# Kernel optimization log

Hardware: AMD Instinct MI355X
Metric: run time of the kernel (lower is better)

## Reference

```python
import jax, jax.numpy as jnp
import numpy as np
from jax import lax

R = 1
EPS = 1e-4
K = 2 * R + 1


def _dir_kernels(r):
    k = 2 * r + 1
    ones = np.ones((k, k), np.float32)
    L = ones.copy(); L[:, r + 1:] = 0
    Rk = ones.copy(); Rk[:, :r] = 0
    U = ones.copy(); U[r + 1:, :] = 0
    D = ones.copy(); D[:r, :] = 0
    # NW/NE/SW/SE clone U/D BEFORE normalization (as in the torch code)
    NW = U.copy(); NW[:, r + 1:] = 0
    NE = U.copy(); NE[:, :r] = 0
    SW = D.copy(); SW[:, r + 1:] = 0
    SE = D.copy(); SE[:, :r] = 0
    half = (r + 1) * k          # normalizer for half windows
    quad = (r + 1) ** 2         # normalizer for quadrant windows
    L, Rk, U, D = L / half, Rk / half, U / half, D / half
    NW, NE, SW, SE = NW / quad, NE / quad, SW / quad, SE / quad
    return jnp.asarray(np.stack([L, Rk, U, D, NW, NE, SW, SE])[:, None])  # [8,1,k,k]


_DN = ('NCHW', 'OIHW', 'NCHW')


def _boxfilter(x, r):
    # replication pad + depthwise ones/(k*k) box filter; x: [N,3,H,W]
    k = 2 * r + 1
    xp = jnp.pad(x, ((0, 0), (0, 0), (r, r), (r, r)), mode='edge')
    w = jnp.full((3, 1, k, k), 1.0 / (k * k), dtype=x.dtype)
    return lax.conv_general_dilated(xp, w, (1, 1), 'VALID',
                                    dimension_numbers=_DN, feature_group_count=3)


def setup_inputs() -> dict:
    key = jax.random.key(0)
    k1, k2, k3 = jax.random.split(key, 3)
    lr_x = jax.random.uniform(k1, (1, 3, 2048, 2048), jnp.float32) * 255.0
    lr_y = jax.random.uniform(k2, (1, 3, 2048, 2048), jnp.float32) * 255.0
    hr_x = jax.random.uniform(k3, (1, 3, 4096, 4096), jnp.float32) * 255.0
    return {"lr_x": lr_x, "lr_y": lr_y, "hr_x": hr_x}


def reference(lr_x, lr_y, hr_x):
    # guided-filter coefficients on the low-res pair
    mean_x = _boxfilter(lr_x, R)
    mean_y = _boxfilter(lr_y, R)
    cov_xy = _boxfilter(lr_x * lr_y, R) - mean_x * mean_y
    var_x = _boxfilter(lr_x * lr_x, R) - mean_x * mean_x
    A = cov_xy / (var_x + EPS)            # [1,3,H,W]
    b = mean_y - A * mean_x               # [1,3,H,W]

    # treat channels as batch: [3,1,H,W]; 8 directional kernels at once
    Wd = _dir_kernels(R)                  # [8,1,k,k]
    A_ = A[0][:, None]
    b_ = b[0][:, None]
    im = lr_x[0][:, None]                 # [3,1,H,W]
    pad = [(R, R), (R, R)]
    convA = lax.conv_general_dilated(A_, Wd, (1, 1), pad, dimension_numbers=_DN)
    convb = lax.conv_general_dilated(b_, Wd, (1, 1), pad, dimension_numbers=_DN)
    d = convA * im + convb - im           # [3,8,H,W] directional residuals

    idx = jnp.argmin(jnp.abs(d), axis=1, keepdims=True)   # [3,1,H,W]
    dm = jnp.take_along_axis(d, idx, axis=1)              # best residual
    res = (dm + im).transpose(1, 0, 2, 3)                 # [1,3,H,W]
    # .int() truncation then clamp to [0,255], back to float
    return jnp.clip(jnp.trunc(res), 0.0, 255.0)
```

## Files before the change

### kernel.cpp

```cpp
#include <hip/hip_runtime.h>
#include <math.h>


#define BX 512
#define TY 16
#define NT 256

__device__ __forceinline__ double fast_rcp(double v) {
#if __has_builtin(__builtin_amdgcn_rcp)
    double r = __builtin_amdgcn_rcp(v);
#else
    double r = 1.0 / v;
#endif
    double e = fma(-v, r, 1.0);
    r = fma(r, e, r);
    e = fma(-v, r, 1.0);
    r = fma(r, e, r);
    return r;
}

__device__ __forceinline__ int iclamp(int v, int lo, int hi) {
    return v < lo ? lo : (v > hi ? hi : v);
}

template <int P, bool EMIT, bool PREF>
__device__ __forceinline__ void fgf_step(
    int S, int y0, int c0, int H, int W,
    const float* __restrict__ xc, const float* __restrict__ yc,
    float* __restrict__ oc,
    const int (&coli)[6], const bool (&av)[4],
    float (&xr)[3][6], float (&yr)[3][6],
    float (&xn)[6], float (&yn)[6],
    double (&CA)[3][2][3], double (&CB)[3][2][3])
{
    const double EPS81 = 81.0 * 1.0e-4;
    const double INV9  = 1.0 / 9.0;
    const double I6    = 1.0 / 6.0;
    constexpr int PO = (P + 1) % 3;
    constexpr int PM = (P + 2) % 3;

#pragma unroll
    for (int k = 0; k < 6; k++) { xr[P][k] = xn[k]; yr[P][k] = yn[k]; }

    if (PREF) {
        int rn = y0 + S + 1; if (rn > H - 1) rn = H - 1;
        const float* __restrict__ pxn = xc + (size_t)rn * W;
        const float* __restrict__ pyn = yc + (size_t)rn * W;
#pragma unroll
        for (int k = 0; k < 6; k++) { xn[k] = pxn[coli[k]]; yn[k] = pyn[coli[k]]; }
    }

    const int ar = y0 + S - 1;

    double Sx[6], Sy[6], Sxy[6], Sxx[6];
#pragma unroll
    for (int k = 0; k < 6; k++) {
        double x0v = (double)xr[PO][k];
        double x1v = (double)xr[PM][k];
        double x2v = (double)xr[P][k];
        double y0v = (double)yr[PO][k];
        double y1v = (double)yr[PM][k];
        double y2v = (double)yr[P][k];
        Sx[k]  = (x0v + x1v) + x2v;
        Sy[k]  = (y0v + y1v) + y2v;
        Sxy[k] = fma(x2v, y2v, fma(x1v, y1v, x0v * y0v));
        Sxx[k] = fma(x2v, x2v, fma(x1v, x1v, x0v * x0v));
    }

    const bool rvalid = (ar >= 0) && (ar < H);
    double Aj[4], Bj[4];
#pragma unroll
    for (int j = 0; j < 4; j++) {
        double sx3  = (Sx[j]  + Sx[j + 1])  + Sx[j + 2];
        double sy3  = (Sy[j]  + Sy[j + 1])  + Sy[j + 2];
        double sxy3 = (Sxy[j] + Sxy[j + 1]) + Sxy[j + 2];
        double sxx3 = (Sxx[j] + Sxx[j + 1]) + Sxx[j + 2];
        double num = fma(9.0, sxy3, -(sx3 * sy3));
        double den = fma(-sx3, sx3, fma(9.0, sxx3, EPS81));
        double Av = num * fast_rcp(den);
        double Bv = fma(-Av, sx3, sy3) * INV9;
        bool ok = rvalid && av[j];
        Aj[j] = ok ? Av : 0.0;
        Bj[j] = ok ? Bv : 0.0;
    }

#pragma unroll
    for (int i = 0; i < 2; i++) {
        double l = Aj[i] + Aj[i + 1], r = Aj[i + 1] + Aj[i + 2];
        CA[P][i][0] = l; CA[P][i][1] = r; CA[P][i][2] = l + Aj[i + 2];
        l = Bj[i] + Bj[i + 1]; r = Bj[i + 1] + Bj[i + 2];
        CB[P][i][0] = l; CB[P][i][1] = r; CB[P][i][2] = l + Bj[i + 2];
    }

    if (EMIT) {
        const int oy = ar - 1;
        if (oy < H) {
            float o0 = 0.0f, o1 = 0.0f;
#pragma unroll
            for (int i = 0; i < 2; i++) {
                double im  = (double)xr[PO][i + 2];
                double mim = -im;
                double nwA = CA[PO][i][0] + CA[PM][i][0];
                double neA = CA[PO][i][1] + CA[PM][i][1];
                double sa[8] = {
                    nwA + CA[P][i][0],
                    neA + CA[P][i][1],
                    CA[PO][i][2] + CA[PM][i][2],
                    CA[PM][i][2] + CA[P][i][2],
                    nwA,
                    neA,
                    CA[PM][i][0] + CA[P][i][0],
                    CA[PM][i][1] + CA[P][i][1]
                };
                double nwB = CB[PO][i][0] + CB[PM][i][0];
                double neB = CB[PO][i][1] + CB[PM][i][1];
                double sb[8] = {
                    nwB + CB[P][i][0],
                    neB + CB[P][i][1],
                    CB[PO][i][2] + CB[PM][i][2],
                    CB[PM][i][2] + CB[P][i][2],
                    nwB,
                    neB,
                    CB[PM][i][0] + CB[P][i][0],
                    CB[PM][i][1] + CB[P][i][1]
                };
                double best = 0.0;
#pragma unroll
                for (int q = 0; q < 8; q++) {
                    double wq = (q < 4) ? I6 : 0.25;
                    double dq = fma(wq, fma(sa[q], im, sb[q]), mim);
                    if (q == 0) best = dq;
                    else best = (fabs(dq) < fabs(best)) ? dq : best;
                }
                double res = trunc(best + im);
                res = fmin(fmax(res, 0.0), 255.0);
                if (i == 0) o0 = (float)res; else o1 = (float)res;
            }
            size_t ob = (size_t)oy * W + c0;
            if (c0 + 1 < W) {
                float2 o2; o2.x = o0; o2.y = o1;
                *reinterpret_cast<float2*>(&oc[ob]) = o2;
            } else if (c0 < W) {
                oc[ob] = o0;
            }
        }
    }
}

__global__ __launch_bounds__(NT, 2) void fgf_band_kernel(
    const float* __restrict__ x, const float* __restrict__ y,
    float* __restrict__ out, int H, int W)
{
    const int c   = blockIdx.z;
    const int bx0 = blockIdx.x * BX;
    const int y0  = blockIdx.y * TY;
    const size_t plane = (size_t)H * (size_t)W;
    const float* xc = x + (size_t)c * plane;
    const float* yc = y + (size_t)c * plane;
    float* oc = out + (size_t)c * plane;

    const int t  = threadIdx.y * 64 + threadIdx.x;
    const int c0 = bx0 + 2 * t;

    int coli[6];
    bool av[4];
#pragma unroll
    for (int k = 0; k < 6; k++) coli[k] = iclamp(c0 - 2 + k, 0, W - 1);
#pragma unroll
    for (int j = 0; j < 4; j++) { int ax = c0 - 1 + j; av[j] = (ax >= 0) && (ax < W); }

    float  xr[3][6], yr[3][6], xn[6], yn[6];
    double CA[3][2][3], CB[3][2][3];

    {
        int r1 = iclamp(y0 - 2, 0, H - 1);
        int r2 = iclamp(y0 - 1, 0, H - 1);
        const float* px1 = xc + (size_t)r1 * W;  const float* py1 = yc + (size_t)r1 * W;
        const float* px2 = xc + (size_t)r2 * W;  const float* py2 = yc + (size_t)r2 * W;
        const float* px3 = xc + (size_t)y0 * W;  const float* py3 = yc + (size_t)y0 * W;
#pragma unroll
        for (int k = 0; k < 6; k++) {
            xr[1][k] = px1[coli[k]]; yr[1][k] = py1[coli[k]];
            xr[2][k] = px2[coli[k]]; yr[2][k] = py2[coli[k]];
            xn[k]    = px3[coli[k]]; yn[k]    = py3[coli[k]];
        }
    }

    fgf_step<0, false, true>(0, y0, c0, H, W, xc, yc, oc, coli, av, xr, yr, xn, yn, CA, CB);
    fgf_step<1, false, true>(1, y0, c0, H, W, xc, yc, oc, coli, av, xr, yr, xn, yn, CA, CB);
#pragma unroll 1
    for (int sb = 0; sb < 5; sb++) {
        const int S2 = 2 + 3 * sb;
        fgf_step<2, true, true>(S2,     y0, c0, H, W, xc, yc, oc, coli, av, xr, yr, xn, yn, CA, CB);
        fgf_step<0, true, true>(S2 + 1, y0, c0, H, W, xc, yc, oc, coli, av, xr, yr, xn, yn, CA, CB);
        fgf_step<1, true, true>(S2 + 2, y0, c0, H, W, xc, yc, oc, coli, av, xr, yr, xn, yn, CA, CB);
    }
    fgf_step<2, true, false>(17, y0, c0, H, W, xc, yc, oc, coli, av, xr, yr, xn, yn, CA, CB);
}

extern "C" void kernel_launch(void* const* d_in, const int* in_sizes, int n_in,
                              void* d_out, int out_size, void* d_ws, size_t ws_size,
                              hipStream_t stream) {
    const float* lr_x = (const float*)d_in[0];
    const float* lr_y = (const float*)d_in[1];
    float* out = (float*)d_out;

    const int plane = in_sizes[0] / 3;
    const int H = (int)(0.5 + sqrt((double)plane));
    const int W = plane / H;

    dim3 block(64, 4, 1);
    dim3 grid((W + BX - 1) / BX, (H + TY - 1) / TY, 3);
    fgf_band_kernel<<<grid, block, 0, stream>>>(lr_x, lr_y, out, H, W);
}
```

Baseline: 348.4 us.

## Map one column per lane and share horizontal sums via DPP row shifts

Each lane now handles a single column, and the horizontal 3-tap sums of the box statistics and the A/B coefficients come from neighbouring lanes through DPP row-shift moves. Before, each thread loaded six columns and recomputed the overlapping sums itself. This removes redundant loads and fp64 arithmetic, but each 64-lane wave emits only 60 output columns because of halo lanes. The band height grows from 16 to 30 rows and the occupancy hint rises to 3, so the redundant halo rows are amortised over more outputs at the cost of more serial work per block.

```diff
diff --git a/kernel.cpp b/kernel.cpp
--- a/kernel.cpp
+++ b/kernel.cpp
@@ -2,8 +2,9 @@
 #include <math.h>
 
 
-#define BX 512
-#define TY 16
+#define WCOLS 60
+#define BCOLS (4 * WCOLS)
+#define TY 30
 #define NT 256
 
 __device__ __forceinline__ double fast_rcp(double v) {
@@ -23,15 +24,25 @@
     return v < lo ? lo : (v > hi ? hi : v);
 }
 
+template <int CTRL>
+__device__ __forceinline__ double dpp_mov64(double v) {
+    int lo = __double2loint(v);
+    int hi = __double2hiint(v);
+    lo = __builtin_amdgcn_mov_dpp(lo, CTRL, 0xF, 0xF, true);
+    hi = __builtin_amdgcn_mov_dpp(hi, CTRL, 0xF, 0xF, true);
+    return __hiloint2double(hi, lo);
+}
+__device__ __forceinline__ double nbr_left(double v)  { return dpp_mov64<0x138>(v); }
+__device__ __forceinline__ double nbr_right(double v) { return dpp_mov64<0x130>(v); }
+
 template <int P, bool EMIT, bool PREF>
 __device__ __forceinline__ void fgf_step(
-    int S, int y0, int c0, int H, int W,
+    int S, int y0, int H, int W,
+    int coli, bool colv, bool outv, int dc,
     const float* __restrict__ xc, const float* __restrict__ yc,
     float* __restrict__ oc,
-    const int (&coli)[6], const bool (&av)[4],
-    float (&xr)[3][6], float (&yr)[3][6],
-    float (&xn)[6], float (&yn)[6],
-    double (&CA)[3][2][3], double (&CB)[3][2][3])
+    double (&X)[3], double (&Y)[3], float& xn, float& yn,
+    double (&CA)[3][3], double (&CB)[3][3])
 {
     const double EPS81 = 81.0 * 1.0e-4;
     const double INV9  = 1.0 / 9.0;
@@ -39,163 +50,139 @@
     constexpr int PO = (P + 1) % 3;
     constexpr int PM = (P + 2) % 3;
 
-#pragma unroll
-    for (int k = 0; k < 6; k++) { xr[P][k] = xn[k]; yr[P][k] = yn[k]; }
+    X[P] = (double)xn;
+    Y[P] = (double)yn;
 
     if (PREF) {
         int rn = y0 + S + 1; if (rn > H - 1) rn = H - 1;
-        const float* __restrict__ pxn = xc + (size_t)rn * W;
-        const float* __restrict__ pyn = yc + (size_t)rn * W;
-#pragma unroll
-        for (int k = 0; k < 6; k++) { xn[k] = pxn[coli[k]]; yn[k] = pyn[coli[k]]; }
+        xn = xc[(size_t)rn * W + coli];
+        yn = yc[(size_t)rn * W + coli];
     }
 
     const int ar = y0 + S - 1;
 
-    double Sx[6], Sy[6], Sxy[6], Sxx[6];
-#pragma unroll
-    for (int k = 0; k < 6; k++) {
-        double x0v = (double)xr[PO][k];
-        double x1v = (double)xr[PM][k];
-        double x2v = (double)xr[P][k];
-        double y0v = (double)yr[PO][k];
-        double y1v = (double)yr[PM][k];
-        double y2v = (double)yr[P][k];
-        Sx[k]  = (x0v + x1v) + x2v;
-        Sy[k]  = (y0v + y1v) + y2v;
-        Sxy[k] = fma(x2v, y2v, fma(x1v, y1v, x0v * y0v));
-        Sxx[k] = fma(x2v, x2v, fma(x1v, x1v, x0v * x0v));
-    }
-
-    const bool rvalid = (ar >= 0) && (ar < H);
-    double Aj[4], Bj[4];
-#pragma unroll
-    for (int j = 0; j < 4; j++) {
-        double sx3  = (Sx[j]  + Sx[j + 1])  + Sx[j + 2];
-        double sy3  = (Sy[j]  + Sy[j + 1])  + Sy[j + 2];
-        double sxy3 = (Sxy[j] + Sxy[j + 1]) + Sxy[j + 2];
-        double sxx3 = (Sxx[j] + Sxx[j + 1]) + Sxx[j + 2];
-        double num = fma(9.0, sxy3, -(sx3 * sy3));
-        double den = fma(-sx3, sx3, fma(9.0, sxx3, EPS81));
-        double Av = num * fast_rcp(den);
-        double Bv = fma(-Av, sx3, sy3) * INV9;
-        bool ok = rvalid && av[j];
-        Aj[j] = ok ? Av : 0.0;
-        Bj[j] = ok ? Bv : 0.0;
-    }
-
-#pragma unroll
-    for (int i = 0; i < 2; i++) {
-        double l = Aj[i] + Aj[i + 1], r = Aj[i + 1] + Aj[i + 2];
-        CA[P][i][0] = l; CA[P][i][1] = r; CA[P][i][2] = l + Aj[i + 2];
-        l = Bj[i] + Bj[i + 1]; r = Bj[i + 1] + Bj[i + 2];
-        CB[P][i][0] = l; CB[P][i][1] = r; CB[P][i][2] = l + Bj[i + 2];
+    double Sx  = (X[PO] + X[PM]) + X[P];
+    double Sy  = (Y[PO] + Y[PM]) + Y[P];
+    double Sxy = fma(X[P], Y[P], fma(X[PM], Y[PM], X[PO] * Y[PO]));
+    double Sxx = fma(X[P], X[P], fma(X[PM], X[PM], X[PO] * X[PO]));
+
+    double Sx3  = (nbr_left(Sx)  + Sx)  + nbr_right(Sx);
+    double Sy3  = (nbr_left(Sy)  + Sy)  + nbr_right(Sy);
+    double Sxy3 = (nbr_left(Sxy) + Sxy) + nbr_right(Sxy);
+    double Sxx3 = (nbr_left(Sxx) + Sxx) + nbr_right(Sxx);
+
+    double num = fma(9.0, Sxy3, -(Sx3 * Sy3));
+    double den = fma(-Sx3, Sx3, fma(9.0, Sxx3, EPS81));
+    double Av = num * fast_rcp(den);
+    double Bv = fma(-Av, Sx3, Sy3) * INV9;
+    bool ok = colv && (ar >= 0) && (ar < H);
+    Av = ok ? Av : 0.0;
+    Bv = ok ? Bv : 0.0;
+
+    double Al = nbr_left(Av), Ar = nbr_right(Av);
+    double Bl = nbr_left(Bv), Br = nbr_right(Bv);
+    {
+        double l = Al + Av, r = Av + Ar;
+        CA[P][0] = l; CA[P][1] = r; CA[P][2] = l + Ar;
+        l = Bl + Bv; r = Bv + Br;
+        CB[P][0] = l; CB[P][1] = r; CB[P][2] = l + Br;
     }
 
     if (EMIT) {
         const int oy = ar - 1;
         if (oy < H) {
-            float o0 = 0.0f, o1 = 0.0f;
+            double im  = X[PO];
+            double mim = -im;
+
+            double nwA = CA[PO][0] + CA[PM][0];
+            double neA = CA[PO][1] + CA[PM][1];
+            double sa[8] = {
+                nwA + CA[P][0],
+                neA + CA[P][1],
+                CA[PO][2] + CA[PM][2],
+                CA[PM][2] + CA[P][2],
+                nwA,
+                neA,
+                CA[PM][0] + CA[P][0],
+                CA[PM][1] + CA[P][1]
+            };
+            double nwB = CB[PO][0] + CB[PM][0];
+            double neB = CB[PO][1] + CB[PM][1];
+            double sb[8] = {
+                nwB + CB[P][0],
+                neB + CB[P][1],
+                CB[PO][2] + CB[PM][2],
+                CB[PM][2] + CB[P][2],
+                nwB,
+                neB,
+                CB[PM][0] + CB[P][0],
+                CB[PM][1] + CB[P][1]
+            };
+
+            double best = 0.0;
 #pragma unroll
-            for (int i = 0; i < 2; i++) {
-                double im  = (double)xr[PO][i + 2];
-                double mim = -im;
-                double nwA = CA[PO][i][0] + CA[PM][i][0];
-                double neA = CA[PO][i][1] + CA[PM][i][1];
-                double sa[8] = {
-                    nwA + CA[P][i][0],
-                    neA + CA[P][i][1],
-                    CA[PO][i][2] + CA[PM][i][2],
-                    CA[PM][i][2] + CA[P][i][2],
-                    nwA,
-                    neA,
-                    CA[PM][i][0] + CA[P][i][0],
-                    CA[PM][i][1] + CA[P][i][1]
-                };
-                double nwB = CB[PO][i][0] + CB[PM][i][0];
-                double neB = CB[PO][i][1] + CB[PM][i][1];
-                double sb[8] = {
-                    nwB + CB[P][i][0],
-                    neB + CB[P][i][1],
-                    CB[PO][i][2] + CB[PM][i][2],
-                    CB[PM][i][2] + CB[P][i][2],
-                    nwB,
-                    neB,
-                    CB[PM][i][0] + CB[P][i][0],
-                    CB[PM][i][1] + CB[P][i][1]
-                };
-                double best = 0.0;
-#pragma unroll
-                for (int q = 0; q < 8; q++) {
-                    double wq = (q < 4) ? I6 : 0.25;
-                    double dq = fma(wq, fma(sa[q], im, sb[q]), mim);
-                    if (q == 0) best = dq;
-                    else best = (fabs(dq) < fabs(best)) ? dq : best;
-                }
-                double res = trunc(best + im);
-                res = fmin(fmax(res, 0.0), 255.0);
-                if (i == 0) o0 = (float)res; else o1 = (float)res;
+            for (int q = 0; q < 8; q++) {
+                double wq = (q < 4) ? I6 : 0.25;
+                double dq = fma(wq, fma(sa[q], im, sb[q]), mim);
+                if (q == 0) best = dq;
+                else best = (fabs(dq) < fabs(best)) ? dq : best;
             }
-            size_t ob = (size_t)oy * W + c0;
-            if (c0 + 1 < W) {
-                float2 o2; o2.x = o0; o2.y = o1;
-                *reinterpret_cast<float2*>(&oc[ob]) = o2;
-            } else if (c0 < W) {
-                oc[ob] = o0;
+
+            double res = trunc(best + im);
+            res = fmin(fmax(res, 0.0), 255.0);
+            if (outv) {
+                oc[(size_t)oy * W + dc] = (float)res;
             }
         }
     }
 }
 
-__global__ __launch_bounds__(NT, 2) void fgf_band_kernel(
+__global__ __launch_bounds__(NT, 3) void fgf_lane_kernel(
     const float* __restrict__ x, const float* __restrict__ y,
     float* __restrict__ out, int H, int W)
 {
     const int c   = blockIdx.z;
-    const int bx0 = blockIdx.x * BX;
     const int y0  = blockIdx.y * TY;
     const size_t plane = (size_t)H * (size_t)W;
     const float* xc = x + (size_t)c * plane;
     const float* yc = y + (size_t)c * plane;
     float* oc = out + (size_t)c * plane;
 
-    const int t  = threadIdx.y * 64 + threadIdx.x;
-    const int c0 = bx0 + 2 * t;
-
-    int coli[6];
-    bool av[4];
-#pragma unroll
-    for (int k = 0; k < 6; k++) coli[k] = iclamp(c0 - 2 + k, 0, W - 1);
-#pragma unroll
-    for (int j = 0; j < 4; j++) { int ax = c0 - 1 + j; av[j] = (ax >= 0) && (ax < W); }
-
-    float  xr[3][6], yr[3][6], xn[6], yn[6];
-    double CA[3][2][3], CB[3][2][3];
+    const int l  = threadIdx.x;
+    const int wv = threadIdx.y;
+    const int out_base = blockIdx.x * BCOLS + wv * WCOLS;
+    const int dc = out_base - 2 + l;
+    const int coli = iclamp(dc, 0, W - 1);
+    const bool colv = (dc >= 0) && (dc < W);
+    const bool outv = (l >= 2) && (l <= 61) && (dc < W);
+
+    double X[3], Y[3];
+    float  xn, yn;
+    double CA[3][3], CB[3][3];
 
     {
         int r1 = iclamp(y0 - 2, 0, H - 1);
         int r2 = iclamp(y0 - 1, 0, H - 1);
-        const float* px1 = xc + (size_t)r1 * W;  const float* py1 = yc + (size_t)r1 * W;
-        const float* px2 = xc + (size_t)r2 * W;  const float* py2 = yc + (size_t)r2 * W;
-        const float* px3 = xc + (size_t)y0 * W;  const float* py3 = yc + (size_t)y0 * W;
-#pragma unroll
-        for (int k = 0; k < 6; k++) {
-            xr[1][k] = px1[coli[k]]; yr[1][k] = py1[coli[k]];
-            xr[2][k] = px2[coli[k]]; yr[2][k] = py2[coli[k]];
-            xn[k]    = px3[coli[k]]; yn[k]    = py3[coli[k]];
-        }
-    }
-
-    fgf_step<0, false, true>(0, y0, c0, H, W, xc, yc, oc, coli, av, xr, yr, xn, yn, CA, CB);
-    fgf_step<1, false, true>(1, y0, c0, H, W, xc, yc, oc, coli, av, xr, yr, xn, yn, CA, CB);
+        X[1] = (double)xc[(size_t)r1 * W + coli];
+        Y[1] = (double)yc[(size_t)r1 * W + coli];
+        X[2] = (double)xc[(size_t)r2 * W + coli];
+        Y[2] = (double)yc[(size_t)r2 * W + coli];
+        xn = xc[(size_t)y0 * W + coli];
+        yn = yc[(size_t)y0 * W + coli];
+    }
+
+    fgf_step<0, false, true>(0, y0, H, W, coli, colv, outv, dc, xc, yc, oc, X, Y, xn, yn, CA, CB);
+    fgf_step<1, false, true>(1, y0, H, W, coli, colv, outv, dc, xc, yc, oc, X, Y, xn, yn, CA, CB);
 #pragma unroll 1
-    for (int sb = 0; sb < 5; sb++) {
+    for (int sb = 0; sb < (TY - 3) / 3; sb++) {
         const int S2 = 2 + 3 * sb;
-        fgf_step<2, true, true>(S2,     y0, c0, H, W, xc, yc, oc, coli, av, xr, yr, xn, yn, CA, CB);
-        fgf_step<0, true, true>(S2 + 1, y0, c0, H, W, xc, yc, oc, coli, av, xr, yr, xn, yn, CA, CB);
-        fgf_step<1, true, true>(S2 + 2, y0, c0, H, W, xc, yc, oc, coli, av, xr, yr, xn, yn, CA, CB);
-    }
-    fgf_step<2, true, false>(17, y0, c0, H, W, xc, yc, oc, coli, av, xr, yr, xn, yn, CA, CB);
+        fgf_step<2, true, true>(S2,     y0, H, W, coli, colv, outv, dc, xc, yc, oc, X, Y, xn, yn, CA, CB);
+        fgf_step<0, true, true>(S2 + 1, y0, H, W, coli, colv, outv, dc, xc, yc, oc, X, Y, xn, yn, CA, CB);
+        fgf_step<1, true, true>(S2 + 2, y0, H, W, coli, colv, outv, dc, xc, yc, oc, X, Y, xn, yn, CA, CB);
+    }
+    fgf_step<2, true, true >(TY - 1, y0, H, W, coli, colv, outv, dc, xc, yc, oc, X, Y, xn, yn, CA, CB);
+    fgf_step<0, true, true >(TY,     y0, H, W, coli, colv, outv, dc, xc, yc, oc, X, Y, xn, yn, CA, CB);
+    fgf_step<1, true, false>(TY + 1, y0, H, W, coli, colv, outv, dc, xc, yc, oc, X, Y, xn, yn, CA, CB);
 }
 
 extern "C" void kernel_launch(void* const* d_in, const int* in_sizes, int n_in,
@@ -210,6 +197,6 @@
     const int W = plane / H;
 
     dim3 block(64, 4, 1);
-    dim3 grid((W + BX - 1) / BX, (H + TY - 1) / TY, 3);
-    fgf_band_kernel<<<grid, block, 0, stream>>>(lr_x, lr_y, out, H, W);
-}
+    dim3 grid((W + BCOLS - 1) / BCOLS, (H + TY - 1) / TY, 3);
+    fgf_lane_kernel<<<grid, block, 0, stream>>>(lr_x, lr_y, out, H, W);
+}
```

Measured after the change: 329.4 us. 1.06x faster.
